# Optimization experiments

Measured on AMD Instinct MI355X. Metric: run time of the kernel, lower is better.

Reference implementation:

```python
import jax, jax.numpy as jnp
import numpy as np

N_NODES = 50000
N_EDGES = 800000
GEN_EPS = 1e-7
LN_EPS = 1e-5


def _mlp3_tanh(x, w0, b0, w1, b1, w2, b2):
    x = jnp.tanh(x @ w0.T + b0)
    x = jnp.tanh(x @ w1.T + b1)
    return jnp.tanh(x @ w2.T + b2)


def _gen_conv(x, src, dst, edge_attr, w0, b0, ln_w, ln_b, w1, b1):
    # GENConv(aggr='softmax', t=1): msg = relu(x_j + e) + eps
    msg = jax.nn.relu(x[src] + edge_attr) + GEN_EPS          # [E, 64]
    m = jax.ops.segment_max(msg, dst, num_segments=N_NODES)  # [N, 64]
    ex = jnp.exp(msg - m[dst])
    den = jax.ops.segment_sum(ex, dst, num_segments=N_NODES)
    alpha = ex / den[dst]                                    # scatter-softmax per dst
    agg = jax.ops.segment_sum(alpha * msg, dst, num_segments=N_NODES)
    h = x + agg                                              # x_r + aggregated messages
    # internal MLP: Linear(64->128), LayerNorm(128), ReLU, Linear(128->64)
    h = h @ w0.T + b0
    mu = jnp.mean(h, axis=-1, keepdims=True)
    var = jnp.mean((h - mu) ** 2, axis=-1, keepdims=True)
    h = ln_w * (h - mu) * jax.lax.rsqrt(var + LN_EPS) + ln_b
    h = jax.nn.relu(h)
    return h @ w1.T + b1


def setup_inputs() -> dict:
    key = jax.random.key(0)
    ks = jax.random.split(key, 32)
    s = 0.05
    d = {
        'node_features': jax.random.normal(ks[0], (N_NODES, 11), jnp.float32),
        'edge_features': jax.random.normal(ks[1], (N_EDGES, 3), jnp.float32),
        'edge_index': jax.random.randint(ks[2], (2, N_EDGES), 0, N_NODES, jnp.int32),
        'ne_w0': jax.random.normal(ks[3], (64, 11)) * s, 'ne_b0': jnp.zeros((64,)),
        'ne_w1': jax.random.normal(ks[4], (64, 64)) * s, 'ne_b1': jnp.zeros((64,)),
        'ne_w2': jax.random.normal(ks[5], (64, 64)) * s, 'ne_b2': jnp.zeros((64,)),
        'ee_w0': jax.random.normal(ks[6], (64, 3)) * s, 'ee_b0': jnp.zeros((64,)),
        'ee_w1': jax.random.normal(ks[7], (64, 64)) * s, 'ee_b1': jnp.zeros((64,)),
        'ee_w2': jax.random.normal(ks[8], (64, 64)) * s, 'ee_b2': jnp.zeros((64,)),
        'mp_w0': jax.random.normal(ks[9], (3, 128, 64)) * s,
        'mp_b0': jnp.zeros((3, 128)),
        'mp_ln_w': jnp.ones((3, 128)), 'mp_ln_b': jnp.zeros((3, 128)),
        'mp_w1': jax.random.normal(ks[10], (3, 64, 128)) * s,
        'mp_b1': jnp.zeros((3, 64)),
        'pi_w0': jax.random.normal(ks[11], (64, 64)) * s, 'pi_b0': jnp.zeros((64,)),
        'pi_w1': jax.random.normal(ks[12], (64, 64)) * s, 'pi_b1': jnp.zeros((64,)),
        'pi_w2': jax.random.normal(ks[13], (2, 64)) * s, 'pi_b2': jnp.zeros((2,)),
    }
    return {k: (v.astype(jnp.float32) if v.dtype != jnp.int32 else v) for k, v in d.items()}


def reference(node_features, edge_features, edge_index,
              ne_w0, ne_b0, ne_w1, ne_b1, ne_w2, ne_b2,
              ee_w0, ee_b0, ee_w1, ee_b1, ee_w2, ee_b2,
              mp_w0, mp_b0, mp_ln_w, mp_ln_b, mp_w1, mp_b1,
              pi_w0, pi_b0, pi_w1, pi_b1, pi_w2, pi_b2):
    src, dst = edge_index[0], edge_index[1]
    x = _mlp3_tanh(node_features, ne_w0, ne_b0, ne_w1, ne_b1, ne_w2, ne_b2)
    e = _mlp3_tanh(edge_features, ee_w0, ee_b0, ee_w1, ee_b1, ee_w2, ee_b2)
    for i in range(3):
        x = _gen_conv(x, src, dst, e, mp_w0[i], mp_b0[i], mp_ln_w[i], mp_ln_b[i], mp_w1[i], mp_b1[i])
    h = jnp.tanh(x @ pi_w0.T + pi_b0)
    h = jnp.tanh(h @ pi_w1.T + pi_b1)
    out = h @ pi_w2.T + pi_b2                 # [N, 2]
    # output.t().reshape(-1)[:n_turbines] == first column of out
    means = -30.0 + (out[:, 0] + 1.0) * 60.0 / 2.0
    return means
```

## Files before the change

### kernel.cpp

```cpp
#include <hip/hip_runtime.h>
#include <hip/hip_fp16.h>
#include <stdint.h>

#define N_NODES 50000
#define N_EDGES 800000
#define SEG 16
#define M_ITEMS (SEG * N_NODES)

typedef unsigned short u16;
typedef unsigned int u32;
typedef __attribute__((ext_vector_type(8))) short short8;
typedef __attribute__((ext_vector_type(4))) float f32x4;
typedef __attribute__((ext_vector_type(4))) u32 u32x4;
typedef __attribute__((ext_vector_type(2))) u32 u32x2;

#define WAVE_SYNC() asm volatile("s_waitcnt lgkmcnt(0)" ::: "memory")

__device__ __forceinline__ float b2f(u16 v) {
    u32 u = ((u32)v) << 16; float f; __builtin_memcpy(&f, &u, 4); return f;
}
__device__ __forceinline__ u16 f2b(float f) {
    u32 u; __builtin_memcpy(&u, &f, 4);
    return (u16)((u + 0x8000u) >> 16);
}
__device__ __forceinline__ float lo2f(u32 p) {
    u32 u = p << 16; float f; __builtin_memcpy(&f, &u, 4); return f;
}
__device__ __forceinline__ float hi2f(u32 p) {
    u32 u = p & 0xffff0000u; float f; __builtin_memcpy(&f, &u, 4); return f;
}
__device__ __forceinline__ u32 pack2(float a, float b) {
    u32 ua, ub; __builtin_memcpy(&ua, &a, 4); __builtin_memcpy(&ub, &b, 4);
    return __builtin_amdgcn_perm(ub + 0x8000u, ua + 0x8000u, 0x07060302u);
}
__device__ __forceinline__ f32x4 mfma16(short8 a, short8 b, f32x4 c) {
    return __builtin_amdgcn_mfma_f32_16x16x32_bf16(a, b, c, 0, 0, 0);
}

__device__ __forceinline__ bool detect_bf(const void* nf) {
    u32 w = ((const u32*)nf)[threadIdx.x & 63];
    u32 lo = w & 0xffffu;
    int e = (int)((lo >> 7) & 0xff);
    int good = ((e >= 118 && e <= 132) || lo == 0) ? 1 : 0;
    unsigned long long b = __ballot(good != 0);
    return __popcll(b) >= 48;
}

#define TANH_TBL_N 256
__device__ __forceinline__ void load_tbl(const u32* __restrict__ g, u32* tbl) {
    int i = (int)threadIdx.x;
    if (i < TANH_TBL_N) tbl[i] = g[i];
    __syncthreads();
}
__device__ __forceinline__ float lut_tanh(const u32* __restrict__ tbl, float x) {
    float a = __builtin_fabsf(x);
    a = fminf(a, 7.96875f);
    int i = (int)(a * 32.f);
    u32 e = tbl[i];
    __half2 h2; __builtin_memcpy(&h2, &e, 4);
    float b = __half2float(__low2half(h2));
    float s = __half2float(__high2half(h2));
    return copysignf(fmaf(s, a, b), x);
}

enum : int {
    NE_B0 = 704,   NE_B1 = 4864,  NE_B2 = 9024,
    EE_B0 = 9280,  EE_B1 = 13440, EE_B2 = 17600,
    MP_B0 = 42240, LNW_O = 42624, LNB_O = 43008, MP_B1 = 67968,
    PI_B0 = 72256, PI_B1 = 76416, PI_W2 = 76480, PI_B2 = 76608,
    W_TOTAL = 76610
};

enum : int {
    FR_EE1 = 0, FR_EE2 = 4, FR_EE3 = 12, FR_NE1 = 20, FR_NE2 = 24, FR_NE3 = 32,
    FR_MP0 = 40, FR_MP1 = 88, FR_PI0 = 136, FR_PI1 = 144, FR_TOTAL = 152
};

#define OFF_W       ((size_t)0)
#define OFF_WB      ((size_t)0x61000)
#define OFF_TBL     ((size_t)0x88000)
#define OFF_XB0     ((size_t)0x90000)
#define OFF_XB1     ((size_t)0x700000)
#define OFF_H64B    ((size_t)0xE00000)
#define OFF_E       ((size_t)0x1500000)
#define OFF_PRA     ((size_t)0x8300000)
#define OFF_CNT16   ((size_t)0x8700000)
#define OFF_CNTT    ((size_t)0x8B00000)
#define OFF_PERM    ((size_t)0x8C00000)
#define OFF_RANK    ((size_t)0x9000000)
#define OFF_SRCS    ((size_t)0x9400000)
#define OFF_BSUM    ((size_t)0x9780000)

struct Ptrs24 { const void* p[24]; };

#define PREP_FRAG   (FR_TOTAL * 512)
#define PREP_BIAS   (PREP_FRAG + 1986)
#define PREP_LUT    (PREP_BIAS + TANH_TBL_N)
#define PREP_TOTAL  (PREP_LUT + M_ITEMS)

__global__ void prep_kernel(const void* nf, Ptrs24 ps, float* __restrict__ W,
                            u16* __restrict__ Wb, u32* __restrict__ gtbl,
                            int* __restrict__ cnt16) {
    bool bf = detect_bf(nf);
    int t = blockIdx.x * blockDim.x + threadIdx.x;
    if (t < PREP_FRAG) {
        const int base[15] = {FR_EE1,FR_EE2,FR_EE3,FR_NE1,FR_NE2,FR_NE3,
                              FR_MP0,FR_MP0+16,FR_MP0+32, FR_MP1,FR_MP1+16,FR_MP1+32,
                              FR_PI0,FR_PI1,FR_TOTAL};
        const int psrc[14]  = {6,8,10, 0,2,4, 12,12,12, 16,16,16, 18,20};
        const int soff[14]  = {0,0,0, 0,0,0, 0,8192,16384, 0,8192,16384, 0,0};
        const int kreal[14] = {3,64,64, 11,64,64, 64,64,64, 128,128,128, 64,64};
        const int nn[14]    = {64,64,64, 64,64,64, 128,128,128, 64,64,64, 64,64};
        int f = t >> 9, r = t & 511, lane = r >> 3, j = r & 7;
        int l = 0;
        while (f >= base[l + 1]) l++;
        int lf = f - base[l];
        int NT = nn[l] >> 4;
        int kt = lf / NT, nt = lf % NT;
        int k = kt * 32 + (lane >> 4) * 8 + j;
        int n = nt * 16 + (lane & 15);
        float v = 0.f;
        if (k < kreal[l]) {
            long idx = (long)soff[l] + (long)n * kreal[l] + k;
            const void* p = ps.p[psrc[l]];
            v = bf ? b2f(((const u16*)p)[idx]) : ((const float*)p)[idx];
        }
        u32 u; __builtin_memcpy(&u, &v, 4);
        Wb[t] = (u16)((u + 0x7fffu + ((u >> 16) & 1u)) >> 16);
        return;
    }
    if (t < PREP_BIAS) {
        int t2 = t - PREP_FRAG;
        const int cnt[14]  = {64,64,64, 64,64,64, 384,384,384,192, 64,64,128,2};
        const int wdst[14] = {NE_B0,NE_B1,NE_B2, EE_B0,EE_B1,EE_B2,
                              MP_B0,LNW_O,LNB_O,MP_B1, PI_B0,PI_B1,PI_W2,PI_B2};
        const int sp[14]   = {1,3,5, 7,9,11, 13,14,15,17, 19,21,22,23};
        int sgi = 0, off = t2;
        while (off >= cnt[sgi]) { off -= cnt[sgi]; sgi++; }
        const void* p = ps.p[sp[sgi]];
        W[wdst[sgi] + off] = bf ? b2f(((const u16*)p)[off]) : ((const float*)p)[off];
        return;
    }
    if (t < PREP_LUT) {
        int i = t - PREP_BIAS;
        float x0 = i * 0.03125f, x1 = x0 + 0.03125f;
        float t0 = tanhf(x0), t1 = tanhf(x1);
        float s = (t1 - t0) * 32.f;
        float b = fmaf(-s, x0, t0);
        __half hs = __float2half(s), hb = __float2half(b);
        u16 us, ub;
        __builtin_memcpy(&us, &hs, 2); __builtin_memcpy(&ub, &hb, 2);
        gtbl[i] = (u32)ub | ((u32)us << 16);
        return;
    }
    if (t < PREP_TOTAL) cnt16[t - PREP_LUT] = 0;
}


__global__ void hist_kernel(const int* __restrict__ dst, int* __restrict__ cnt16,
                            int* __restrict__ rank) {
    int e = blockIdx.x * blockDim.x + threadIdx.x;
    if (e >= N_EDGES) return;
    int g = e >> 16;
    rank[e] = atomicAdd(&cnt16[dst[e] * SEG + g], 1);
}

__global__ void padfix_kernel(int* __restrict__ cnt16, int* __restrict__ cntTot) {
    int d = blockIdx.x * blockDim.x + threadIdx.x;
    if (d >= N_NODES) return;
    int C = 0;
#pragma unroll
    for (int g = 0; g < SEG; g++) C += cnt16[d * SEG + g];
    cntTot[d] = C;
    if (C & 1) cnt16[d * SEG + SEG - 1] += 1;
}

__global__ void scanA(const int* __restrict__ cnt16, int* __restrict__ pra,
                      int* __restrict__ bsum) {
    __shared__ int wsum[16];
    int tid = threadIdx.x, lane = tid & 63, wid = tid >> 6;
    int i0 = blockIdx.x * 2048 + tid * 2;
    int v0 = (i0 >= 1 && i0 <= M_ITEMS) ? cnt16[i0 - 1] : 0;
    int v1 = (i0 + 1 <= M_ITEMS) ? cnt16[i0] : 0;
    int v = v0 + v1;
#pragma unroll
    for (int off = 1; off < 64; off <<= 1) {
        int t = __shfl_up(v, off, 64);
        if (lane >= off) v += t;
    }
    if (lane == 63) wsum[wid] = v;
    __syncthreads();
    if (tid == 0) { int a = 0; for (int w = 0; w < 16; w++) { a += wsum[w]; wsum[w] = a; } }
    __syncthreads();
    int incl = v + (wid ? wsum[wid - 1] : 0);
    if (i0 <= M_ITEMS) pra[i0] = incl - v1;
    if (i0 + 1 <= M_ITEMS) pra[i0 + 1] = incl;
    if (tid == 1023) bsum[blockIdx.x] = incl;
}

__global__ void scanB(int* __restrict__ bsum, int nb) {
    int lane = (int)threadIdx.x;
    int carry = 0;
    for (int base = 0; base < nb; base += 64) {
        int v = (base + lane < nb) ? bsum[base + lane] : 0;
#pragma unroll
        for (int off = 1; off < 64; off <<= 1) {
            int t = __shfl_up(v, off, 64);
            if (lane >= off) v += t;
        }
        int tot = __shfl(v, 63, 64);
        if (base + lane < nb) bsum[base + lane] = v + carry;
        carry += tot;
    }
}

__global__ void scanC(const int* __restrict__ bsum, const int* __restrict__ cntTot,
                      int* __restrict__ pra, int* __restrict__ srcs) {
    int i = blockIdx.x * 1024 + threadIdx.x;
    if (i > M_ITEMS) return;
    int b = i >> 11;
    int v = pra[i] + (b ? bsum[b - 1] : 0);
    pra[i] = v;
    if (i < M_ITEMS && (i & (SEG - 1)) == 0) {
        int d = i / SEG;
        int C = cntTot[d];
        if (C & 1) srcs[v + C] = -1;
    }
}

__global__ void scatter_kernel(const int* __restrict__ dst, const int* __restrict__ src,
                               const int* __restrict__ rank, const int* __restrict__ pra,
                               int* __restrict__ perm, int* __restrict__ srcs) {
    int e = blockIdx.x * blockDim.x + threadIdx.x;
    if (e >= N_EDGES) return;
    int g = e >> 16;
    int p = pra[dst[e] * SEG + g] + rank[e];
    perm[e] = p;
    srcs[p] = src[e];
}


template<int KT, int NT, int INSTR>
__device__ __forceinline__ void mfma_layer(const u32* ldsin, int lane,
        const short8* __restrict__ Wf, int basef, const float* __restrict__ bias, f32x4* acc) {
    int q = lane >> 4, mr = lane & 15;
#pragma unroll
    for (int nt = 0; nt < NT; nt++) acc[nt] = *(const f32x4*)(bias + nt * 16 + q * 4);
#pragma unroll
    for (int kt = 0; kt < KT; kt++) {
        short8 act = *(const short8*)(ldsin + mr * INSTR + kt * 16 + q * 4);
#pragma unroll
        for (int nt = 0; nt < NT; nt++)
            acc[nt] = mfma16(Wf[(basef + kt * NT + nt) * 64 + lane], act, acc[nt]);
    }
}

template<int KT, int NT>
__device__ __forceinline__ void mfma_layer_reg(const short8* act, int lane,
        const short8* __restrict__ Wf, int basef, const float* __restrict__ bias, f32x4* acc) {
    int q = lane >> 4;
#pragma unroll
    for (int nt = 0; nt < NT; nt++) acc[nt] = *(const f32x4*)(bias + nt * 16 + q * 4);
#pragma unroll
    for (int kt = 0; kt < KT; kt++)
#pragma unroll
        for (int nt = 0; nt < NT; nt++)
            acc[nt] = mfma16(Wf[(basef + kt * NT + nt) * 64 + lane], act[kt], acc[nt]);
}

template<int NT, int OUTSTR>
__device__ __forceinline__ void tanh_pack_lds(const f32x4* acc, u32* ldsout, int lane,
                                              const u32* __restrict__ tbl) {
    int q = lane >> 4, mr = lane & 15;
#pragma unroll
    for (int nt = 0; nt < NT; nt++) {
        f32x4 a = acc[nt];
        u32x2 pb;
        pb.x = pack2(lut_tanh(tbl, a[0]), lut_tanh(tbl, a[1]));
        pb.y = pack2(lut_tanh(tbl, a[2]), lut_tanh(tbl, a[3]));
        *(u32x2*)&ldsout[mr * OUTSTR + nt * 8 + q * 2] = pb;
    }
}

__device__ __forceinline__ void zero_stage(u32* B0, int lane) {
#pragma unroll
    for (int it = 0; it < 4; it++) {
        int f = lane + 64 * it;
        B0[(f >> 4) * 36 + (f & 15)] = 0;
    }
}


#define EDGE_SPLIT_BLOCKS (N_EDGES / 128)

__global__ __launch_bounds__(256) void edge_encoder(const void* nf, const void* ef,
        u32* __restrict__ ebuf, const int* __restrict__ perm, const float* __restrict__ W,
        const short8* __restrict__ Wf, const u32* __restrict__ gtbl, int part) {
    __shared__ u32 lds[4 * 1152];
    __shared__ u32 tbl[TANH_TBL_N];
    bool bf = detect_bf(nf);
    load_tbl(gtbl, tbl);
    int wv = threadIdx.x >> 6, lane = threadIdx.x & 63;
    u32* B0 = lds + wv * 1152;
    u32* B1 = B0 + 576;
    long ebase = ((long)blockIdx.x + (long)part * EDGE_SPLIT_BLOCKS) * 64 + wv * 16;
    zero_stage(B0, lane);
    if (lane < 16) {
        long e = ebase + lane;
        float i0, i1, i2;
        if (bf) { const u16* p = (const u16*)ef + e * 3; i0 = b2f(p[0]); i1 = b2f(p[1]); i2 = b2f(p[2]); }
        else    { const float* p = (const float*)ef + e * 3; i0 = p[0]; i1 = p[1]; i2 = p[2]; }
        u32* row = B0 + lane * 36;
        row[0] = pack2(i0, i1); row[1] = pack2(i2, 0.f);
    }
    WAVE_SYNC();
    f32x4 acc[4];
    mfma_layer<1, 4, 36>(B0, lane, Wf, FR_EE1, W + EE_B0, acc);
    tanh_pack_lds<4, 36>(acc, B1, lane, tbl);
    WAVE_SYNC();
    mfma_layer<2, 4, 36>(B1, lane, Wf, FR_EE2, W + EE_B1, acc);
    tanh_pack_lds<4, 36>(acc, B0, lane, tbl);
    WAVE_SYNC();
    mfma_layer<2, 4, 36>(B0, lane, Wf, FR_EE3, W + EE_B2, acc);
    tanh_pack_lds<4, 36>(acc, B1, lane, tbl);
    WAVE_SYNC();
    int ro = lane >> 2, cc = (lane & 3) * 8;
    long e = ebase + ro;
    long prowp = perm[e];
    u32x4 v0 = *(const u32x4*)&B1[ro * 36 + cc];
    u32x4 v1 = *(const u32x4*)&B1[ro * 36 + cc + 4];
    *(u32x4*)&ebuf[prowp * 32 + cc] = v0;
    *(u32x4*)&ebuf[prowp * 32 + cc + 4] = v1;
}

__global__ __launch_bounds__(256) void node_encoder(const void* nf,
        u16* __restrict__ xbf, const float* __restrict__ W,
        const short8* __restrict__ Wf, const u32* __restrict__ gtbl) {
    __shared__ u32 lds[4 * 1152];
    __shared__ u32 tbl[TANH_TBL_N];
    bool bf = detect_bf(nf);
    load_tbl(gtbl, tbl);
    int wv = threadIdx.x >> 6, lane = threadIdx.x & 63;
    int q = lane >> 4, mr = lane & 15;
    u32* B0 = lds + wv * 1152;
    u32* B1 = B0 + 576;
    long nbase = (long)blockIdx.x * 64 + wv * 16;
    zero_stage(B0, lane);
    if (lane < 16) {
        long n = nbase + lane;
        if (n < N_NODES) {
            float in[11];
#pragma unroll
            for (int j = 0; j < 11; j++)
                in[j] = bf ? b2f(((const u16*)nf)[n * 11 + j]) : ((const float*)nf)[n * 11 + j];
            u32* row = B0 + lane * 36;
#pragma unroll
            for (int d = 0; d < 5; d++) row[d] = pack2(in[2 * d], in[2 * d + 1]);
            row[5] = pack2(in[10], 0.f);
        }
    }
    WAVE_SYNC();
    f32x4 acc[4];
    mfma_layer<1, 4, 36>(B0, lane, Wf, FR_NE1, W + NE_B0, acc);
    tanh_pack_lds<4, 36>(acc, B1, lane, tbl);
    WAVE_SYNC();
    mfma_layer<2, 4, 36>(B1, lane, Wf, FR_NE2, W + NE_B1, acc);
    tanh_pack_lds<4, 36>(acc, B0, lane, tbl);
    WAVE_SYNC();
    mfma_layer<2, 4, 36>(B0, lane, Wf, FR_NE3, W + NE_B2, acc);
    long n = nbase + mr;
    if (n < N_NODES) {
#pragma unroll
        for (int nt = 0; nt < 4; nt++) {
            u32x2 pb;
            pb.x = pack2(lut_tanh(tbl, acc[nt][0]), lut_tanh(tbl, acc[nt][1]));
            pb.y = pack2(lut_tanh(tbl, acc[nt][2]), lut_tanh(tbl, acc[nt][3]));
            *(u32x2*)&xbf[n * 64 + nt * 16 + q * 4] = pb;
        }
    }
}

#define AGG_HALF_WAVES (N_NODES / 4)
template<int R>
__global__ __launch_bounds__(256) void aggregate_kernel(
        const u32* __restrict__ xbf32, const u32* __restrict__ ebuf32,
        const int* __restrict__ srcs, const int* __restrict__ pra,
        u32* __restrict__ h64bf32, int part) {
    __shared__ int ldsW[4][64];
    int wv = threadIdx.x >> 6;
    int wid = (int)((blockIdx.x * 256 + threadIdx.x) >> 6) + part * AGG_HALF_WAVES;
    int lane = (int)(threadIdx.x & 63);
    int n0 = __builtin_amdgcn_readfirstlane(wid) * 2;
    if (n0 >= N_NODES) return;
    int qt = lane >> 4, h16 = lane & 15;
    int rl = n0 + (lane < 2 ? lane : 2);
    int rv = pra[rl * SEG];
    int kb0 = __shfl(rv, 0, 64);
    int kb1 = __shfl(rv, 1, 64);
    int kb2 = __shfl(rv, 2, 64);
    float an[2][4], ad[2][4];
#pragma unroll
    for (int j = 0; j < 2; j++)
#pragma unroll
        for (int f = 0; f < 4; f++) { an[j][f] = 0.f; ad[j][f] = 0.f; }
    for (int wb = kb0; wb < kb2; wb += 64) {
        ldsW[wv][lane] = srcs[wb + lane];
        WAVE_SYNC();
        int we = wb + 64;
        int hi0 = kb1 < we ? kb1 : we;
        int lo1 = kb1 > wb ? kb1 : wb;
        int hi1 = kb2 < we ? kb2 : we;
#pragma unroll 2
        for (int k = wb; k < hi0; k += 4) {
            int e = k + qt;
            int eoc = (e < hi0) ? e : (hi0 - 1);
            int s = ldsW[wv][eoc - wb];
            u32x2 ev = *(const u32x2*)&ebuf32[(size_t)eoc * 32 + 2 * h16];
            u32x2 xv = *(const u32x2*)&xbf32[(size_t)(s > 0 ? s : 0) * 32 + 2 * h16];
            float vf = (e < hi0 && s >= 0) ? 1.f : 0.f;
            float m0 = fmaxf(lo2f(xv.x) + lo2f(ev.x), 0.f) + 1e-7f;
            float m1 = fmaxf(hi2f(xv.x) + hi2f(ev.x), 0.f) + 1e-7f;
            float m2 = fmaxf(lo2f(xv.y) + lo2f(ev.y), 0.f) + 1e-7f;
            float m3 = fmaxf(hi2f(xv.y) + hi2f(ev.y), 0.f) + 1e-7f;
            float w0 = __expf(m0) * vf, w1 = __expf(m1) * vf;
            float w2 = __expf(m2) * vf, w3 = __expf(m3) * vf;
            an[0][0] = fmaf(w0, m0, an[0][0]); ad[0][0] += w0;
            an[0][1] = fmaf(w1, m1, an[0][1]); ad[0][1] += w1;
            an[0][2] = fmaf(w2, m2, an[0][2]); ad[0][2] += w2;
            an[0][3] = fmaf(w3, m3, an[0][3]); ad[0][3] += w3;
        }
#pragma unroll 2
        for (int k = lo1; k < hi1; k += 4) {
            int e = k + qt;
            int eoc = (e < hi1) ? e : (hi1 - 1);
            int s = ldsW[wv][eoc - wb];
            u32x2 ev = *(const u32x2*)&ebuf32[(size_t)eoc * 32 + 2 * h16];
            u32x2 xv = *(const u32x2*)&xbf32[(size_t)(s > 0 ? s : 0) * 32 + 2 * h16];
            float vf = (e < hi1 && s >= 0) ? 1.f : 0.f;
            float m0 = fmaxf(lo2f(xv.x) + lo2f(ev.x), 0.f) + 1e-7f;
            float m1 = fmaxf(hi2f(xv.x) + hi2f(ev.x), 0.f) + 1e-7f;
            float m2 = fmaxf(lo2f(xv.y) + lo2f(ev.y), 0.f) + 1e-7f;
            float m3 = fmaxf(hi2f(xv.y) + hi2f(ev.y), 0.f) + 1e-7f;
            float w0 = __expf(m0) * vf, w1 = __expf(m1) * vf;
            float w2 = __expf(m2) * vf, w3 = __expf(m3) * vf;
            an[1][0] = fmaf(w0, m0, an[1][0]); ad[1][0] += w0;
            an[1][1] = fmaf(w1, m1, an[1][1]); ad[1][1] += w1;
            an[1][2] = fmaf(w2, m2, an[1][2]); ad[1][2] += w2;
            an[1][3] = fmaf(w3, m3, an[1][3]); ad[1][3] += w3;
        }
        WAVE_SYNC();
    }
#pragma unroll
    for (int j = 0; j < 2; j++) {
#pragma unroll
        for (int f = 0; f < 4; f++) {
            an[j][f] += __shfl_xor(an[j][f], 16, 64);
            an[j][f] += __shfl_xor(an[j][f], 32, 64);
            ad[j][f] += __shfl_xor(ad[j][f], 16, 64);
            ad[j][f] += __shfl_xor(ad[j][f], 32, 64);
        }
        if (qt == 0) {
            float a0 = (ad[j][0] > 0.f) ? __fdividef(an[j][0], ad[j][0]) : 0.f;
            float a1 = (ad[j][1] > 0.f) ? __fdividef(an[j][1], ad[j][1]) : 0.f;
            float a2 = (ad[j][2] > 0.f) ? __fdividef(an[j][2], ad[j][2]) : 0.f;
            float a3 = (ad[j][3] > 0.f) ? __fdividef(an[j][3], ad[j][3]) : 0.f;
            u32x2 xr = *(const u32x2*)&xbf32[(size_t)(n0 + j) * 32 + 2 * h16];
            u32x2 o;
            o.x = pack2(lo2f(xr.x) + a0, hi2f(xr.x) + a1);
            o.y = pack2(lo2f(xr.y) + a2, hi2f(xr.y) + a3);
            *(u32x2*)&h64bf32[(size_t)(n0 + j) * 32 + 2 * h16] = o;
        }
    }
}

__global__ __launch_bounds__(256) void mlp_fused(const u16* __restrict__ h64bf,
        u16* __restrict__ xbf,
        const float* __restrict__ W, const short8* __restrict__ Wf, int r) {
    __shared__ u32 lds[4 * 1088];
    int wv = threadIdx.x >> 6, lane = threadIdx.x & 63;
    int q = lane >> 4, mr = lane & 15;
    u32* bufY = lds + wv * 1088;
    long nbase = (long)blockIdx.x * 64 + wv * 16;
    long row = nbase + mr;
    long rc = (row < N_NODES) ? row : (N_NODES - 1);
    short8 act[2];
#pragma unroll
    for (int kt = 0; kt < 2; kt++)
        act[kt] = *(const short8*)&h64bf[rc * 64 + kt * 32 + q * 8];
    f32x4 acc[8];
    mfma_layer_reg<2, 8>(act, lane, Wf, FR_MP0 + r * 16, W + MP_B0 + r * 128, acc);
    float s = 0.f, sq = 0.f;
#pragma unroll
    for (int nt = 0; nt < 8; nt++)
#pragma unroll
        for (int rr = 0; rr < 4; rr++) { float v = acc[nt][rr]; s += v; sq = fmaf(v, v, sq); }
    s += __shfl_xor(s, 16, 64);  s += __shfl_xor(s, 32, 64);
    sq += __shfl_xor(sq, 16, 64); sq += __shfl_xor(sq, 32, 64);
    float mu = s * (1.f / 128.f);
    float var = sq * (1.f / 128.f) - mu * mu;
    float inv = rsqrtf(var + 1e-5f);
    const float* LW = W + LNW_O + r * 128;
    const float* LB = W + LNB_O + r * 128;
#pragma unroll
    for (int nt = 0; nt < 8; nt++) {
        f32x4 lw = *(const f32x4*)(LW + nt * 16 + q * 4);
        f32x4 lb = *(const f32x4*)(LB + nt * 16 + q * 4);
        float u0 = fmaxf(fmaf((acc[nt][0] - mu) * inv, lw[0], lb[0]), 0.f);
        float u1 = fmaxf(fmaf((acc[nt][1] - mu) * inv, lw[1], lb[1]), 0.f);
        float u2 = fmaxf(fmaf((acc[nt][2] - mu) * inv, lw[2], lb[2]), 0.f);
        float u3 = fmaxf(fmaf((acc[nt][3] - mu) * inv, lw[3], lb[3]), 0.f);
        u32x2 pb; pb.x = pack2(u0, u1); pb.y = pack2(u2, u3);
        *(u32x2*)&bufY[mr * 68 + nt * 8 + q * 2] = pb;
    }
    WAVE_SYNC();
    f32x4 acc2[4];
    mfma_layer<4, 4, 68>(bufY, lane, Wf, FR_MP1 + r * 16, W + MP_B1 + r * 64, acc2);
    if (row < N_NODES) {
#pragma unroll
        for (int nt = 0; nt < 4; nt++) {
            f32x4 v = acc2[nt];
            u32x2 pb; pb.x = pack2(v[0], v[1]); pb.y = pack2(v[2], v[3]);
            *(u32x2*)&xbf[row * 64 + nt * 16 + q * 4] = pb;
        }
    }
}

__global__ __launch_bounds__(256) void policy_head(const void* nf,
        const u16* __restrict__ xbf, void* out, const float* __restrict__ W,
        const short8* __restrict__ Wf, const u32* __restrict__ gtbl) {
    __shared__ u32 lds[4 * 576];
    __shared__ u32 tbl[TANH_TBL_N];
    bool bf = detect_bf(nf);
    load_tbl(gtbl, tbl);
    int wv = threadIdx.x >> 6, lane = threadIdx.x & 63;
    int q = lane >> 4, mr = lane & 15;
    u32* bufY = lds + wv * 576;
    long nbase = (long)blockIdx.x * 64 + wv * 16;
    long row = nbase + mr;
    long rc = (row < N_NODES) ? row : (N_NODES - 1);
    short8 act[2];
#pragma unroll
    for (int kt = 0; kt < 2; kt++)
        act[kt] = *(const short8*)&xbf[rc * 64 + kt * 32 + q * 8];
    f32x4 acc[4];
    mfma_layer_reg<2, 4>(act, lane, Wf, FR_PI0, W + PI_B0, acc);
    tanh_pack_lds<4, 36>(acc, bufY, lane, tbl);
    WAVE_SYNC();
    mfma_layer<2, 4, 36>(bufY, lane, Wf, FR_PI1, W + PI_B1, acc);
    float o = 0.f;
#pragma unroll
    for (int nt = 0; nt < 4; nt++) {
        f32x4 w2 = *(const f32x4*)(W + PI_W2 + nt * 16 + q * 4);
#pragma unroll
        for (int rr = 0; rr < 4; rr++) o = fmaf(lut_tanh(tbl, acc[nt][rr]), w2[rr], o);
    }
    o += __shfl_xor(o, 16, 64);
    o += __shfl_xor(o, 32, 64);
    if (lane < 16 && row < N_NODES) {
        float means = 30.f * (o + W[PI_B2]);
        if (bf) ((u16*)out)[row] = f2b(means);
        else    ((float*)out)[row] = means;
    }
}

extern "C" void kernel_launch(void* const* d_in, const int* in_sizes, int n_in,
                              void* d_out, int out_size, void* d_ws, size_t ws_size,
                              hipStream_t stream) {
    char* ws = (char*)d_ws;
    float* W      = (float*)(ws + OFF_W);
    u16*   Wb     = (u16*)(ws + OFF_WB);
    const short8* Wf = (const short8*)(ws + OFF_WB);
    u32*   gtbl   = (u32*)(ws + OFF_TBL);
    u16*   xb0    = (u16*)(ws + OFF_XB0);
    u16*   xb1    = (u16*)(ws + OFF_XB1);
    u16*   h64bf  = (u16*)(ws + OFF_H64B);
    u32*   h64b32 = (u32*)(ws + OFF_H64B);
    u32*   ebuf32 = (u32*)(ws + OFF_E);
    int*   pra    = (int*)(ws + OFF_PRA);
    int*   cnt16  = (int*)(ws + OFF_CNT16);
    int*   cntTot = (int*)(ws + OFF_CNTT);
    int*   perm   = (int*)(ws + OFF_PERM);
    int*   rank   = (int*)(ws + OFF_RANK);
    int*   srcs   = (int*)(ws + OFF_SRCS);
    int*   bsum   = (int*)(ws + OFF_BSUM);

    const void* nf  = d_in[0];
    const int* ei   = (const int*)d_in[2];
    const int* srcv = ei;
    const int* dstv = ei + N_EDGES;

    Ptrs24 ps;
    for (int k = 0; k < 24; k++) ps.p[k] = d_in[3 + k];
    prep_kernel<<<(PREP_TOTAL + 255) / 256, 256, 0, stream>>>(nf, ps, W, Wb, gtbl, cnt16);

    hist_kernel<<<(N_EDGES + 255) / 256, 256, 0, stream>>>(dstv, cnt16, rank);
    padfix_kernel<<<(N_NODES + 255) / 256, 256, 0, stream>>>(cnt16, cntTot);
    const int scanABlocks = (M_ITEMS + 1 + 2047) / 2048;
    scanA<<<scanABlocks, 1024, 0, stream>>>(cnt16, pra, bsum);
    scanB<<<1, 64, 0, stream>>>(bsum, scanABlocks);
    scanC<<<(M_ITEMS + 1024) / 1024, 1024, 0, stream>>>(bsum, cntTot, pra, srcs);
    scatter_kernel<<<(N_EDGES + 255) / 256, 256, 0, stream>>>(dstv, srcv, rank, pra, perm, srcs);

    node_encoder<<<(N_NODES + 63) / 64, 256, 0, stream>>>(nf, xb0, W, Wf, gtbl);
    edge_encoder<<<EDGE_SPLIT_BLOCKS, 256, 0, stream>>>(nf, d_in[1], ebuf32, perm, W, Wf, gtbl, 0);
    edge_encoder<<<EDGE_SPLIT_BLOCKS, 256, 0, stream>>>(nf, d_in[1], ebuf32, perm, W, Wf, gtbl, 1);

    u16* xbc = xb0; u16* xbn = xb1;
    const int aggHalfBlocks = AGG_HALF_WAVES / 4;
    aggregate_kernel<0><<<aggHalfBlocks, 256, 0, stream>>>((const u32*)xbc, ebuf32, srcs, pra, h64b32, 0);
    aggregate_kernel<0><<<aggHalfBlocks, 256, 0, stream>>>((const u32*)xbc, ebuf32, srcs, pra, h64b32, 1);
    mlp_fused<<<(N_NODES + 63) / 64, 256, 0, stream>>>(h64bf, xbn, W, Wf, 0);
    { u16* tb = xbc; xbc = xbn; xbn = tb; }
    aggregate_kernel<1><<<aggHalfBlocks, 256, 0, stream>>>((const u32*)xbc, ebuf32, srcs, pra, h64b32, 0);
    aggregate_kernel<1><<<aggHalfBlocks, 256, 0, stream>>>((const u32*)xbc, ebuf32, srcs, pra, h64b32, 1);
    mlp_fused<<<(N_NODES + 63) / 64, 256, 0, stream>>>(h64bf, xbn, W, Wf, 1);
    { u16* tb = xbc; xbc = xbn; xbn = tb; }
    aggregate_kernel<2><<<aggHalfBlocks, 256, 0, stream>>>((const u32*)xbc, ebuf32, srcs, pra, h64b32, 0);
    aggregate_kernel<2><<<aggHalfBlocks, 256, 0, stream>>>((const u32*)xbc, ebuf32, srcs, pra, h64b32, 1);
    mlp_fused<<<(N_NODES + 63) / 64, 256, 0, stream>>>(h64bf, xbn, W, Wf, 2);
    { u16* tb = xbc; xbc = xbn; xbn = tb; }

    policy_head<<<(N_NODES + 63) / 64, 256, 0, stream>>>(nf, xbc, d_out, W, Wf, gtbl);
}
```

Measured before the change: 417.3 us.

## Widen aggregate gathers to 16-byte loads and merge split launches

The aggregation kernel now has each lane load 16 bytes (8 bf16 features) per edge instead of 8 bytes. That puts 8 edges per wave iteration instead of 4, with an extra shuffle-reduce stage across octets. The next 64-edge window of source indices is prefetched into a register while the current one is processed. The two half-launches per layer are merged into one launch, cutting launch overhead. The costs are higher register use, since the accumulators double, and a possible read past the end of srcs by the prefetch.

```diff
diff --git a/kernel.cpp b/kernel.cpp
--- a/kernel.cpp
+++ b/kernel.cpp
@@ -380,95 +380,96 @@
     }
 }
 
-#define AGG_HALF_WAVES (N_NODES / 4)
 template<int R>
 __global__ __launch_bounds__(256) void aggregate_kernel(
         const u32* __restrict__ xbf32, const u32* __restrict__ ebuf32,
         const int* __restrict__ srcs, const int* __restrict__ pra,
-        u32* __restrict__ h64bf32, int part) {
+        u32* __restrict__ h64bf32) {
     __shared__ int ldsW[4][64];
     int wv = threadIdx.x >> 6;
-    int wid = (int)((blockIdx.x * 256 + threadIdx.x) >> 6) + part * AGG_HALF_WAVES;
+    int wid = (int)((blockIdx.x * 256 + threadIdx.x) >> 6);
     int lane = (int)(threadIdx.x & 63);
     int n0 = __builtin_amdgcn_readfirstlane(wid) * 2;
     if (n0 >= N_NODES) return;
-    int qt = lane >> 4, h16 = lane & 15;
+    int oct = lane >> 3, h8 = lane & 7;
     int rl = n0 + (lane < 2 ? lane : 2);
     int rv = pra[rl * SEG];
     int kb0 = __shfl(rv, 0, 64);
     int kb1 = __shfl(rv, 1, 64);
     int kb2 = __shfl(rv, 2, 64);
-    float an[2][4], ad[2][4];
+    float an[2][8], ad[2][8];
 #pragma unroll
     for (int j = 0; j < 2; j++)
 #pragma unroll
-        for (int f = 0; f < 4; f++) { an[j][f] = 0.f; ad[j][f] = 0.f; }
+        for (int f = 0; f < 8; f++) { an[j][f] = 0.f; ad[j][f] = 0.f; }
+    int pre = srcs[kb0 + lane];
     for (int wb = kb0; wb < kb2; wb += 64) {
-        ldsW[wv][lane] = srcs[wb + lane];
+        ldsW[wv][lane] = pre;
         WAVE_SYNC();
+        pre = srcs[wb + 64 + lane];
         int we = wb + 64;
         int hi0 = kb1 < we ? kb1 : we;
         int lo1 = kb1 > wb ? kb1 : wb;
         int hi1 = kb2 < we ? kb2 : we;
 #pragma unroll 2
-        for (int k = wb; k < hi0; k += 4) {
-            int e = k + qt;
+        for (int k = wb; k < hi0; k += 8) {
+            int e = k + oct;
             int eoc = (e < hi0) ? e : (hi0 - 1);
             int s = ldsW[wv][eoc - wb];
-            u32x2 ev = *(const u32x2*)&ebuf32[(size_t)eoc * 32 + 2 * h16];
-            u32x2 xv = *(const u32x2*)&xbf32[(size_t)(s > 0 ? s : 0) * 32 + 2 * h16];
+            u32x4 ev = *(const u32x4*)&ebuf32[(size_t)eoc * 32 + 4 * h8];
+            u32x4 xv = *(const u32x4*)&xbf32[(size_t)(s > 0 ? s : 0) * 32 + 4 * h8];
             float vf = (e < hi0 && s >= 0) ? 1.f : 0.f;
-            float m0 = fmaxf(lo2f(xv.x) + lo2f(ev.x), 0.f) + 1e-7f;
-            float m1 = fmaxf(hi2f(xv.x) + hi2f(ev.x), 0.f) + 1e-7f;
-            float m2 = fmaxf(lo2f(xv.y) + lo2f(ev.y), 0.f) + 1e-7f;
-            float m3 = fmaxf(hi2f(xv.y) + hi2f(ev.y), 0.f) + 1e-7f;
-            float w0 = __expf(m0) * vf, w1 = __expf(m1) * vf;
-            float w2 = __expf(m2) * vf, w3 = __expf(m3) * vf;
-            an[0][0] = fmaf(w0, m0, an[0][0]); ad[0][0] += w0;
-            an[0][1] = fmaf(w1, m1, an[0][1]); ad[0][1] += w1;
-            an[0][2] = fmaf(w2, m2, an[0][2]); ad[0][2] += w2;
-            an[0][3] = fmaf(w3, m3, an[0][3]); ad[0][3] += w3;
+#pragma unroll
+            for (int c = 0; c < 4; c++) {
+                float m0 = fmaxf(lo2f(xv[c]) + lo2f(ev[c]), 0.f) + 1e-7f;
+                float m1 = fmaxf(hi2f(xv[c]) + hi2f(ev[c]), 0.f) + 1e-7f;
+                float w0 = __expf(m0) * vf, w1 = __expf(m1) * vf;
+                an[0][2 * c]     = fmaf(w0, m0, an[0][2 * c]);     ad[0][2 * c]     += w0;
+                an[0][2 * c + 1] = fmaf(w1, m1, an[0][2 * c + 1]); ad[0][2 * c + 1] += w1;
+            }
         }
 #pragma unroll 2
-        for (int k = lo1; k < hi1; k += 4) {
-            int e = k + qt;
+        for (int k = lo1; k < hi1; k += 8) {
+            int e = k + oct;
             int eoc = (e < hi1) ? e : (hi1 - 1);
             int s = ldsW[wv][eoc - wb];
-            u32x2 ev = *(const u32x2*)&ebuf32[(size_t)eoc * 32 + 2 * h16];
-            u32x2 xv = *(const u32x2*)&xbf32[(size_t)(s > 0 ? s : 0) * 32 + 2 * h16];
+            u32x4 ev = *(const u32x4*)&ebuf32[(size_t)eoc * 32 + 4 * h8];
+            u32x4 xv = *(const u32x4*)&xbf32[(size_t)(s > 0 ? s : 0) * 32 + 4 * h8];
             float vf = (e < hi1 && s >= 0) ? 1.f : 0.f;
-            float m0 = fmaxf(lo2f(xv.x) + lo2f(ev.x), 0.f) + 1e-7f;
-            float m1 = fmaxf(hi2f(xv.x) + hi2f(ev.x), 0.f) + 1e-7f;
-            float m2 = fmaxf(lo2f(xv.y) + lo2f(ev.y), 0.f) + 1e-7f;
-            float m3 = fmaxf(hi2f(xv.y) + hi2f(ev.y), 0.f) + 1e-7f;
-            float w0 = __expf(m0) * vf, w1 = __expf(m1) * vf;
-            float w2 = __expf(m2) * vf, w3 = __expf(m3) * vf;
-            an[1][0] = fmaf(w0, m0, an[1][0]); ad[1][0] += w0;
-            an[1][1] = fmaf(w1, m1, an[1][1]); ad[1][1] += w1;
-            an[1][2] = fmaf(w2, m2, an[1][2]); ad[1][2] += w2;
-            an[1][3] = fmaf(w3, m3, an[1][3]); ad[1][3] += w3;
+#pragma unroll
+            for (int c = 0; c < 4; c++) {
+                float m0 = fmaxf(lo2f(xv[c]) + lo2f(ev[c]), 0.f) + 1e-7f;
+                float m1 = fmaxf(hi2f(xv[c]) + hi2f(ev[c]), 0.f) + 1e-7f;
+                float w0 = __expf(m0) * vf, w1 = __expf(m1) * vf;
+                an[1][2 * c]     = fmaf(w0, m0, an[1][2 * c]);     ad[1][2 * c]     += w0;
+                an[1][2 * c + 1] = fmaf(w1, m1, an[1][2 * c + 1]); ad[1][2 * c + 1] += w1;
+            }
         }
         WAVE_SYNC();
     }
 #pragma unroll
     for (int j = 0; j < 2; j++) {
 #pragma unroll
-        for (int f = 0; f < 4; f++) {
+        for (int f = 0; f < 8; f++) {
+            an[j][f] += __shfl_xor(an[j][f], 8, 64);
             an[j][f] += __shfl_xor(an[j][f], 16, 64);
             an[j][f] += __shfl_xor(an[j][f], 32, 64);
+            ad[j][f] += __shfl_xor(ad[j][f], 8, 64);
             ad[j][f] += __shfl_xor(ad[j][f], 16, 64);
             ad[j][f] += __shfl_xor(ad[j][f], 32, 64);
         }
-        if (qt == 0) {
-            float a0 = (ad[j][0] > 0.f) ? __fdividef(an[j][0], ad[j][0]) : 0.f;
-            float a1 = (ad[j][1] > 0.f) ? __fdividef(an[j][1], ad[j][1]) : 0.f;
-            float a2 = (ad[j][2] > 0.f) ? __fdividef(an[j][2], ad[j][2]) : 0.f;
-            float a3 = (ad[j][3] > 0.f) ? __fdividef(an[j][3], ad[j][3]) : 0.f;
-            u32x2 xr = *(const u32x2*)&xbf32[(size_t)(n0 + j) * 32 + 2 * h16];
-            u32x2 o;
-            o.x = pack2(lo2f(xr.x) + a0, hi2f(xr.x) + a1);
-            o.y = pack2(lo2f(xr.y) + a2, hi2f(xr.y) + a3);
-            *(u32x2*)&h64bf32[(size_t)(n0 + j) * 32 + 2 * h16] = o;
+        if (oct == 0) {
+            float a[8];
+#pragma unroll
+            for (int f = 0; f < 8; f++)
+                a[f] = (ad[j][f] > 0.f) ? __fdividef(an[j][f], ad[j][f]) : 0.f;
+            u32x4 xr = *(const u32x4*)&xbf32[(size_t)(n0 + j) * 32 + 4 * h8];
+            u32x4 o;
+            o.x = pack2(lo2f(xr.x) + a[0], hi2f(xr.x) + a[1]);
+            o.y = pack2(lo2f(xr.y) + a[2], hi2f(xr.y) + a[3]);
+            o.z = pack2(lo2f(xr.z) + a[4], hi2f(xr.z) + a[5]);
+            o.w = pack2(lo2f(xr.w) + a[6], hi2f(xr.w) + a[7]);
+            *(u32x4*)&h64bf32[(size_t)(n0 + j) * 32 + 4 * h8] = o;
         }
     }
 }
@@ -606,17 +607,14 @@
     edge_encoder<<<EDGE_SPLIT_BLOCKS, 256, 0, stream>>>(nf, d_in[1], ebuf32, perm, W, Wf, gtbl, 1);
 
     u16* xbc = xb0; u16* xbn = xb1;
-    const int aggHalfBlocks = AGG_HALF_WAVES / 4;
-    aggregate_kernel<0><<<aggHalfBlocks, 256, 0, stream>>>((const u32*)xbc, ebuf32, srcs, pra, h64b32, 0);
-    aggregate_kernel<0><<<aggHalfBlocks, 256, 0, stream>>>((const u32*)xbc, ebuf32, srcs, pra, h64b32, 1);
+    const int aggBlocks = (N_NODES / 2 * 64) / 256;
+    aggregate_kernel<0><<<aggBlocks, 256, 0, stream>>>((const u32*)xbc, ebuf32, srcs, pra, h64b32);
     mlp_fused<<<(N_NODES + 63) / 64, 256, 0, stream>>>(h64bf, xbn, W, Wf, 0);
     { u16* tb = xbc; xbc = xbn; xbn = tb; }
-    aggregate_kernel<1><<<aggHalfBlocks, 256, 0, stream>>>((const u32*)xbc, ebuf32, srcs, pra, h64b32, 0);
-    aggregate_kernel<1><<<aggHalfBlocks, 256, 0, stream>>>((const u32*)xbc, ebuf32, srcs, pra, h64b32, 1);
+    aggregate_kernel<1><<<aggBlocks, 256, 0, stream>>>((const u32*)xbc, ebuf32, srcs, pra, h64b32);
     mlp_fused<<<(N_NODES + 63) / 64, 256, 0, stream>>>(h64bf, xbn, W, Wf, 1);
     { u16* tb = xbc; xbc = xbn; xbn = tb; }
-    aggregate_kernel<2><<<aggHalfBlocks, 256, 0, stream>>>((const u32*)xbc, ebuf32, srcs, pra, h64b32, 0);
-    aggregate_kernel<2><<<aggHalfBlocks, 256, 0, stream>>>((const u32*)xbc, ebuf32, srcs, pra, h64b32, 1);
+    aggregate_kernel<2><<<aggBlocks, 256, 0, stream>>>((const u32*)xbc, ebuf32, srcs, pra, h64b32);
     mlp_fused<<<(N_NODES + 63) / 64, 256, 0, stream>>>(h64bf, xbn, W, Wf, 2);
     { u16* tb = xbc; xbc = xbn; xbn = tb; }
 
```

Measured after the change: 423.5 us. About the same (+1.5%).
